# Performance work log

Hardware: AMD Instinct MI355X
Metric: run time of the kernel (lower is better)

## Reference

```python
import jax, jax.numpy as jnp
import numpy as np

B, L, D = 2, 2048, 2048
HEADS, DIM_HEAD = 16, 128
INNER = HEADS * DIM_HEAD
EPS = 1e-6


def _rmsnorm(x, w):
    # RMSNorm over last dim, matching nn.RMSNorm(inner_dim, eps)
    return x * jax.lax.rsqrt(jnp.mean(x * x, axis=-1, keepdims=True) + EPS) * w


def _rope_interleaved(x, cos, sin):
    # x: [B, L, INNER]; cos/sin: [1, L, INNER//2]
    x1 = x[..., 0::2]
    x2 = x[..., 1::2]
    o1 = x1 * cos - x2 * sin
    o2 = x1 * sin + x2 * cos
    return jnp.stack([o1, o2], axis=-1).reshape(x.shape)


def setup_inputs() -> dict:
    key = jax.random.key(0)
    ks = jax.random.split(key, 16)
    s = 0.02
    inp = {
        "x": jax.random.normal(ks[0], (B, L, D), jnp.float32),
        "pe_cos": jax.random.normal(ks[1], (1, L, INNER // 2), jnp.float32),
        "pe_sin": jax.random.normal(ks[2], (1, L, INNER // 2), jnp.float32),
        "logit_log_scale": jax.random.uniform(ks[3], (1, L, 1), jnp.float32),
        "wq": jax.random.normal(ks[4], (D, INNER), jnp.float32) * s,
        "bq": jnp.zeros((INNER,), jnp.float32),
        "wk": jax.random.normal(ks[5], (D, INNER), jnp.float32) * s,
        "bk": jnp.zeros((INNER,), jnp.float32),
        "wv": jax.random.normal(ks[6], (D, INNER), jnp.float32) * s,
        "bv": jnp.zeros((INNER,), jnp.float32),
        "qn_w": jnp.ones((INNER,), jnp.float32),
        "kn_w": jnp.ones((INNER,), jnp.float32),
        "wo": jax.random.normal(ks[7], (INNER, D), jnp.float32) * s,
        "bo": jnp.zeros((D,), jnp.float32),
    }
    return inp


def reference(x, pe_cos, pe_sin, logit_log_scale, wq, bq, wk, bk, wv, bv, qn_w, kn_w, wo, bo):
    # QKV projections
    q = _rmsnorm(x @ wq + bq, qn_w)
    k = _rmsnorm(x @ wk + bk, kn_w)
    v = x @ wv + bv
    # Interleaved RoPE on flattened inner dim
    q = _rope_interleaved(q, pe_cos, pe_sin)
    k = _rope_interleaved(k, pe_cos, pe_sin)
    # Position-dependent logit temperature applied to Q
    q = q * logit_log_scale
    # Split heads: [B, L, H, Dh]
    q = q.reshape(B, L, HEADS, DIM_HEAD)
    k = k.reshape(B, L, HEADS, DIM_HEAD)
    v = v.reshape(B, L, HEADS, DIM_HEAD)
    scale = 1.0 / jnp.sqrt(jnp.asarray(DIM_HEAD, jnp.float32))
    scores = jnp.einsum("bqhd,bkhd->bhqk", q, k) * scale  # [B, H, L, L]
    causal = jnp.tril(jnp.ones((L, L), bool))
    scores = jnp.where(causal[None, None], scores, jnp.asarray(-1e30, scores.dtype))
    attn = jax.nn.softmax(scores, axis=-1)
    out = jnp.einsum("bhqk,bkhd->bqhd", attn, v).reshape(B, L, INNER)
    return out @ wo + bo
```

## Files before the change

kernel.cpp:

```cpp
#include <hip/hip_runtime.h>
#include <hip/hip_bf16.h>

typedef __bf16 bf16x8_t __attribute__((ext_vector_type(8)));
typedef float  f32x4_t  __attribute__((ext_vector_type(4)));

#define B_     2
#define L_     2048
#define D_     2048
#define H_     16
#define DH_    128
#define INNER_ 2048
#define M_     (B_ * L_)

__device__ __forceinline__ void gld_lds16(const void* g, void* l) {
    __builtin_amdgcn_global_load_lds(
        (const __attribute__((address_space(1))) void*)g,
        (__attribute__((address_space(3))) void*)l,
        16, 0, 0);
}

__device__ __forceinline__ unsigned short f2bf(float f) {
    __hip_bfloat16 h = __float2bfloat16(f);
    return *(unsigned short*)&h;
}
__device__ __forceinline__ float bf2f(unsigned short s) {
    return __uint_as_float(((unsigned)s) << 16);
}

__global__ __launch_bounds__(256)
void k_cast(const float* __restrict__ in, unsigned short* __restrict__ out) {
    const size_t i = ((size_t)blockIdx.x * 256 + threadIdx.x) * 4;
    float4 v = *(const float4*)(in + i);
    ushort4 o;
    o.x = f2bf(v.x); o.y = f2bf(v.y); o.z = f2bf(v.z); o.w = f2bf(v.w);
    *(ushort4*)(out + i) = o;
}

__global__ __launch_bounds__(256)
void k_transpose_cast(const float* __restrict__ in, unsigned short* __restrict__ out) {
    __shared__ unsigned short tile[32][33];
    const int t  = threadIdx.x;
    const int r  = t >> 3;
    const int c4 = (t & 7) << 2;
    const size_t ib = ((size_t)blockIdx.y * 32 + r) * 2048 + blockIdx.x * 32 + c4;
    float4 v = *(const float4*)(in + ib);
    tile[r][c4 + 0] = f2bf(v.x); tile[r][c4 + 1] = f2bf(v.y);
    tile[r][c4 + 2] = f2bf(v.z); tile[r][c4 + 3] = f2bf(v.w);
    __syncthreads();
    ushort4 o;
    o.x = tile[c4 + 0][r]; o.y = tile[c4 + 1][r];
    o.z = tile[c4 + 2][r]; o.w = tile[c4 + 3][r];
    const size_t ob = ((size_t)blockIdx.x * 32 + r) * 2048 + blockIdx.y * 32 + c4;
    *(ushort4*)(out + ob) = o;
}

__global__ __launch_bounds__(256)
void k_transpose2048(const unsigned short* __restrict__ in,
                     unsigned short* __restrict__ out) {
    __shared__ unsigned short tile[32][33];
    const int t  = threadIdx.x;
    const int r  = t >> 3;
    const int c4 = (t & 7) << 2;
    const size_t ib = ((size_t)blockIdx.y * 32 + r) * 2048 + blockIdx.x * 32 + c4;
    ushort4 v = *(const ushort4*)(in + ib);
    tile[r][c4 + 0] = v.x; tile[r][c4 + 1] = v.y;
    tile[r][c4 + 2] = v.z; tile[r][c4 + 3] = v.w;
    __syncthreads();
    ushort4 o;
    o.x = tile[c4 + 0][r]; o.y = tile[c4 + 1][r];
    o.z = tile[c4 + 2][r]; o.w = tile[c4 + 3][r];
    const size_t ob = ((size_t)blockIdx.x * 32 + r) * 2048 + blockIdx.y * 32 + c4;
    *(ushort4*)(out + ob) = o;
}

#define GEMM_BODY(A_, Bt_, K_)                                                 \
    __shared__ __align__(16) __hip_bfloat16 As[128 * 32];                      \
    __shared__ __align__(16) __hip_bfloat16 Bs[128 * 32];                      \
    const int t    = threadIdx.x;                                              \
    const int lane = t & 63;                                                   \
    const int wave = t >> 6;                                                   \
    const int quad = lane >> 4;                                                \
    const int l16  = lane & 15;                                                \
    const int wm   = (wave >> 1) * 64;                                         \
    const int wn   = (wave & 1) * 64;                                          \
    const int srow = t >> 2;                                                   \
    const int scol = (t & 3) << 3;                                             \
    const __hip_bfloat16* Ag = A_  + (size_t)(tileM + srow) * K_ + scol;       \
    const __hip_bfloat16* Bg = Bt_ + (size_t)(tileN + srow) * K_ + scol;       \
    __hip_bfloat16* Asl  = &As[t * 8];                                         \
    __hip_bfloat16* Asl2 = &As[2048 + t * 8];                                  \
    __hip_bfloat16* Bsl  = &Bs[t * 8];                                         \
    __hip_bfloat16* Bsl2 = &Bs[2048 + t * 8];                                  \
    const size_t rowskip = (size_t)64 * K_;                                    \
    f32x4_t acc[4][4];                                                         \
    _Pragma("unroll") for (int i = 0; i < 4; i++)                              \
        _Pragma("unroll") for (int j = 0; j < 4; j++)                          \
            acc[i][j] = (f32x4_t){0.f, 0.f, 0.f, 0.f};                         \
    for (int k0 = 0; k0 < K_; k0 += 32) {                                      \
        __syncthreads();                                                       \
        gld_lds16(Ag + k0,           Asl);                                     \
        gld_lds16(Ag + rowskip + k0, Asl2);                                    \
        gld_lds16(Bg + k0,           Bsl);                                     \
        gld_lds16(Bg + rowskip + k0, Bsl2);                                    \
        __syncthreads();                                                       \
        bf16x8_t af[4], bfr[4];                                                \
        _Pragma("unroll") for (int i = 0; i < 4; i++)                          \
            af[i] = *(const bf16x8_t*)&As[(wm + i * 16 + l16) * 32 + quad * 8];\
        _Pragma("unroll") for (int j = 0; j < 4; j++)                          \
            bfr[j] = *(const bf16x8_t*)&Bs[(wn + j * 16 + l16) * 32 + quad * 8];\
        _Pragma("unroll") for (int i = 0; i < 4; i++)                          \
            _Pragma("unroll") for (int j = 0; j < 4; j++)                      \
                acc[i][j] = __builtin_amdgcn_mfma_f32_16x16x32_bf16(           \
                    af[i], bfr[j], acc[i][j], 0, 0, 0);                        \
    }

__global__ __launch_bounds__(256)
void k_gemm_bt_f32(const __hip_bfloat16* __restrict__ A,
                   const __hip_bfloat16* __restrict__ Bt,
                   const float* __restrict__ bias,
                   float* __restrict__ C,
                   int M, int N, int K) {
    const int tileM = blockIdx.x * 128;
    const int tileN = blockIdx.y * 128;
    GEMM_BODY(A, Bt, K)
#pragma unroll
    for (int i = 0; i < 4; i++)
#pragma unroll
        for (int r = 0; r < 4; r++) {
            const int m = tileM + wm + i * 16 + quad * 4 + r;
#pragma unroll
            for (int j = 0; j < 4; j++) {
                const int n = tileN + wn + j * 16 + l16;
                C[(size_t)m * N + n] = acc[i][j][r] + bias[n];
            }
        }
}

__global__ __launch_bounds__(256)
void k_gemm_qkv(const __hip_bfloat16* __restrict__ A,
                const __hip_bfloat16* __restrict__ Bt,
                const float* __restrict__ bq, const float* __restrict__ bk,
                const float* __restrict__ bv,
                __hip_bfloat16* __restrict__ qo, __hip_bfloat16* __restrict__ ko,
                __hip_bfloat16* __restrict__ vo) {
    const int tileM = blockIdx.x * 128;
    const int tileN = blockIdx.y * 128;
    GEMM_BODY(A, Bt, D_)
    const int sel  = blockIdx.y >> 4;
    const int nbas = tileN - sel * INNER_;
    const float* bias = (sel == 0) ? bq : (sel == 1) ? bk : bv;
    __hip_bfloat16* C = (sel == 0) ? qo : (sel == 1) ? ko : vo;
#pragma unroll
    for (int i = 0; i < 4; i++)
#pragma unroll
        for (int r = 0; r < 4; r++) {
            const int m = tileM + wm + i * 16 + quad * 4 + r;
#pragma unroll
            for (int j = 0; j < 4; j++) {
                const int n = nbas + wn + j * 16 + l16;
                C[(size_t)m * INNER_ + n] = __float2bfloat16(acc[i][j][r] + bias[n]);
            }
        }
}

__global__ __launch_bounds__(256)
void k_rmsrope(__hip_bfloat16* __restrict__ buf,
               const float* __restrict__ w,
               const float* __restrict__ pcos,
               const float* __restrict__ psin,
               const float* __restrict__ lls,
               float extra) {
    const int row = blockIdx.x;
    const int l   = row & (L_ - 1);
    const int t   = threadIdx.x;
    __hip_bfloat16* p = buf + (size_t)row * INNER_ + t * 8;

    float x[8];
    {
        const unsigned short* ps = (const unsigned short*)p;
        ushort4 a = *(const ushort4*)ps;
        ushort4 b = *(const ushort4*)(ps + 4);
        unsigned short s[8] = {a.x, a.y, a.z, a.w, b.x, b.y, b.z, b.w};
#pragma unroll
        for (int i = 0; i < 8; i++) x[i] = bf2f(s[i]);
    }
    float ss = 0.f;
#pragma unroll
    for (int i = 0; i < 8; i++) ss += x[i] * x[i];
#pragma unroll
    for (int off = 32; off >= 1; off >>= 1) ss += __shfl_down(ss, off);
    __shared__ float red[4];
    if ((t & 63) == 0) red[t >> 6] = ss;
    __syncthreads();
    ss = red[0] + red[1] + red[2] + red[3];
    const float rstd = rsqrtf(ss * (1.0f / (float)INNER_) + 1e-6f);

    float scale = extra;
    if (lls) scale *= lls[l];

    const float4 c4 = ((const float4*)(pcos + (size_t)l * (INNER_ / 2)))[t];
    const float4 s4 = ((const float4*)(psin + (size_t)l * (INNER_ / 2)))[t];
    const float cc[4] = {c4.x, c4.y, c4.z, c4.w};
    const float sn[4] = {s4.x, s4.y, s4.z, s4.w};
    const float4 w0 = ((const float4*)w)[t * 2];
    const float4 w1 = ((const float4*)w)[t * 2 + 1];
    const float ww[8] = {w0.x, w0.y, w0.z, w0.w, w1.x, w1.y, w1.z, w1.w};

    union { __hip_bfloat16 h[8]; uint4 u; } pk;
#pragma unroll
    for (int pi = 0; pi < 4; pi++) {
        const float y1 = x[pi * 2]     * rstd * ww[pi * 2];
        const float y2 = x[pi * 2 + 1] * rstd * ww[pi * 2 + 1];
        pk.h[pi * 2]     = __float2bfloat16((y1 * cc[pi] - y2 * sn[pi]) * scale);
        pk.h[pi * 2 + 1] = __float2bfloat16((y1 * sn[pi] + y2 * cc[pi]) * scale);
    }
    *(uint4*)p = pk.u;
}

__global__ __launch_bounds__(256)
void k_attn(const __hip_bfloat16* __restrict__ q,
            const __hip_bfloat16* __restrict__ k,
            const __hip_bfloat16* __restrict__ vT,
            __hip_bfloat16* __restrict__ o) {
    __shared__ __align__(16) __hip_bfloat16 Ks[64 * 128];
    __shared__ __align__(16) __hip_bfloat16 Vs[128 * 64];
    __shared__ __align__(16) __hip_bfloat16 Ps[4][16 * 72];

    const int p  = blockIdx.x;
    const int bh = blockIdx.y;
    const int b  = bh >> 4;
    const int h  = bh & 15;
    const int t = threadIdx.x, wave = t >> 6, lane = t & 63;
    const int quad = lane >> 4, l16 = lane & 15;

    const int krow = t >> 4;
    const int kcol = ((t & 15) ^ krow) << 3;
    const int vrow = t >> 3;
    const int vcol = ((t & 7) ^ (vrow & 7)) << 3;

    for (int half = 0; half < 2; ++half) {
        const int qt = half ? (31 - p) : p;

        bf16x8_t aq[4];
        {
            const size_t qoff = (size_t)(b * L_ + qt * 64 + wave * 16 + l16) * INNER_ + h * DH_;
#pragma unroll
            for (int kk = 0; kk < 4; kk++)
                aq[kk] = *(const bf16x8_t*)(q + qoff + kk * 32 + quad * 8);
        }

        f32x4_t oacc[8];
#pragma unroll
        for (int jj = 0; jj < 8; jj++) oacc[jj] = (f32x4_t){0.f, 0.f, 0.f, 0.f};
        float mrow[4] = {-1e30f, -1e30f, -1e30f, -1e30f};
        float lrow[4] = {0.f, 0.f, 0.f, 0.f};

        for (int kt = 0; kt <= qt; ++kt) {
            const int kv0 = kt * 64;
            __syncthreads();
#pragma unroll
            for (int i = 0; i < 4; i++) {
                gld_lds16(k  + (size_t)(b * L_ + kv0 + i * 16 + krow) * INNER_ + h * DH_ + kcol,
                          &Ks[t * 8 + i * 2048]);
                gld_lds16(vT + ((size_t)bh * DH_ + i * 32 + vrow) * L_ + kv0 + vcol,
                          &Vs[t * 8 + i * 2048]);
            }
            __syncthreads();

            f32x4_t sacc[4];
#pragma unroll
            for (int j = 0; j < 4; j++) sacc[j] = (f32x4_t){0.f, 0.f, 0.f, 0.f};
#pragma unroll
            for (int j = 0; j < 4; j++)
#pragma unroll
                for (int kk = 0; kk < 4; kk++) {
                    bf16x8_t bk_ = *(const bf16x8_t*)
                        &Ks[(j * 16 + l16) * 128 + (((kk * 4 + quad) ^ l16) << 3)];
                    sacc[j] = __builtin_amdgcn_mfma_f32_16x16x32_bf16(aq[kk], bk_, sacc[j], 0, 0, 0);
                }

            if (kt == qt) {
                const int qbase = qt * 64 + wave * 16 + quad * 4;
#pragma unroll
                for (int j = 0; j < 4; j++) {
                    const int key = kv0 + j * 16 + l16;
#pragma unroll
                    for (int r = 0; r < 4; r++)
                        if (key > qbase + r) sacc[j][r] = -1e30f;
                }
            }

            float alpha[4];
#pragma unroll
            for (int r = 0; r < 4; r++) {
                float mx = fmaxf(fmaxf(sacc[0][r], sacc[1][r]), fmaxf(sacc[2][r], sacc[3][r]));
#pragma unroll
                for (int off = 1; off < 16; off <<= 1) mx = fmaxf(mx, __shfl_xor(mx, off));
                const float mnew = fmaxf(mrow[r], mx);
                alpha[r] = exp2f(mrow[r] - mnew);
                float s0 = 0.f;
#pragma unroll
                for (int j = 0; j < 4; j++) {
                    const float pv = exp2f(sacc[j][r] - mnew);
                    Ps[wave][(quad * 4 + r) * 72 + j * 16 + l16] = __float2bfloat16(pv);
                    s0 += pv;
                }
#pragma unroll
                for (int off = 1; off < 16; off <<= 1) s0 += __shfl_xor(s0, off);
                lrow[r] = lrow[r] * alpha[r] + s0;
                mrow[r] = mnew;
            }

#pragma unroll
            for (int jj = 0; jj < 8; jj++)
#pragma unroll
                for (int r = 0; r < 4; r++) oacc[jj][r] *= alpha[r];

#pragma unroll
            for (int kk2 = 0; kk2 < 2; kk2++) {
                bf16x8_t ap = *(const bf16x8_t*)&Ps[wave][l16 * 72 + kk2 * 32 + quad * 8];
#pragma unroll
                for (int jj = 0; jj < 8; jj++) {
                    bf16x8_t bv_ = *(const bf16x8_t*)
                        &Vs[(jj * 16 + l16) * 64 + (((kk2 * 4 + quad) ^ (l16 & 7)) << 3)];
                    oacc[jj] = __builtin_amdgcn_mfma_f32_16x16x32_bf16(ap, bv_, oacc[jj], 0, 0, 0);
                }
            }
        }

#pragma unroll
        for (int r = 0; r < 4; r++) {
            const int qi = qt * 64 + wave * 16 + quad * 4 + r;
            const float inv = 1.0f / lrow[r];
#pragma unroll
            for (int jj = 0; jj < 8; jj++) {
                const int d = jj * 16 + l16;
                o[(size_t)(b * L_ + qi) * INNER_ + h * DH_ + d] =
                    __float2bfloat16(oacc[jj][r] * inv);
            }
        }
    }
}

extern "C" void kernel_launch(void* const* d_in, const int* in_sizes, int n_in,
                              void* d_out, int out_size, void* d_ws, size_t ws_size,
                              hipStream_t stream) {
    const float* x      = (const float*)d_in[0];
    const float* pe_cos = (const float*)d_in[1];
    const float* pe_sin = (const float*)d_in[2];
    const float* lls    = (const float*)d_in[3];
    const float* wq     = (const float*)d_in[4];
    const float* bq     = (const float*)d_in[5];
    const float* wk     = (const float*)d_in[6];
    const float* bk     = (const float*)d_in[7];
    const float* wv     = (const float*)d_in[8];
    const float* bv     = (const float*)d_in[9];
    const float* qn     = (const float*)d_in[10];
    const float* kn     = (const float*)d_in[11];
    const float* wo     = (const float*)d_in[12];
    const float* bo     = (const float*)d_in[13];

    char* ws = (char*)d_ws;
    const size_t SZ_W = (size_t)D_ * INNER_ * 2;
    const size_t SZ_M = (size_t)M_ * INNER_ * 2;
    __hip_bfloat16* xb     = (__hip_bfloat16*)ws;  ws += SZ_M;
    __hip_bfloat16* wqkvT  = (__hip_bfloat16*)ws;  ws += 3 * SZ_W;
    __hip_bfloat16* woT    = (__hip_bfloat16*)ws;  ws += SZ_W;
    __hip_bfloat16* qb     = (__hip_bfloat16*)ws;  ws += SZ_M;
    __hip_bfloat16* kb     = (__hip_bfloat16*)ws;  ws += SZ_M;
    __hip_bfloat16* vb     = (__hip_bfloat16*)ws;  ws += SZ_M;
    __hip_bfloat16* vT     = (__hip_bfloat16*)ws;  ws += SZ_M;
    __hip_bfloat16* ab     = (__hip_bfloat16*)ws;  ws += SZ_M;
    (void)in_sizes; (void)n_in; (void)out_size; (void)ws_size;

    const dim3 tb(256);
    const dim3 gT(64, 64);

    k_cast<<<(M_ * D_) / 1024, tb, 0, stream>>>(x, (unsigned short*)xb);

    k_transpose_cast<<<gT, tb, 0, stream>>>(wq, (unsigned short*)(wqkvT));
    k_transpose_cast<<<gT, tb, 0, stream>>>(wk, (unsigned short*)(wqkvT + (size_t)INNER_ * D_));
    k_transpose_cast<<<gT, tb, 0, stream>>>(wv, (unsigned short*)(wqkvT + 2 * (size_t)INNER_ * D_));
    k_transpose_cast<<<gT, tb, 0, stream>>>(wo, (unsigned short*)woT);

    k_gemm_qkv<<<dim3(M_ / 128, 48), tb, 0, stream>>>(xb, wqkvT, bq, bk, bv, qb, kb, vb);

    const float qextra = 0.08838834764831843f  * 1.4426950408889634f ;
    k_rmsrope<<<M_, tb, 0, stream>>>(qb, qn, pe_cos, pe_sin, lls, qextra);
    k_rmsrope<<<M_, tb, 0, stream>>>(kb, kn, pe_cos, pe_sin, nullptr, 1.0f);

    k_transpose2048<<<gT, tb, 0, stream>>>((const unsigned short*)vb, (unsigned short*)vT);
    k_transpose2048<<<gT, tb, 0, stream>>>((const unsigned short*)(vb + (size_t)L_ * INNER_),
                                           (unsigned short*)(vT + (size_t)L_ * INNER_));

    k_attn<<<dim3(16, B_ * H_), tb, 0, stream>>>(qb, kb, vT, ab);

    k_gemm_bt_f32<<<dim3(M_ / 128, D_ / 128), tb, 0, stream>>>(ab, woT, bo, (float*)d_out, M_, D_, INNER_);
}
```

Measured before the change: 476.3 us.

## Enlarge attention query tile to 128 rows with transposed MFMA operand layout

```diff
diff --git a/kernel.cpp b/kernel.cpp
--- a/kernel.cpp
+++ b/kernel.cpp
@@ -224,7 +224,7 @@
             __hip_bfloat16* __restrict__ o) {
     __shared__ __align__(16) __hip_bfloat16 Ks[64 * 128];
     __shared__ __align__(16) __hip_bfloat16 Vs[128 * 64];
-    __shared__ __align__(16) __hip_bfloat16 Ps[4][16 * 72];
+    __shared__ __align__(16) __hip_bfloat16 Pt[8][16 * 72];
 
     const int p  = blockIdx.x;
     const int bh = blockIdx.y;
@@ -233,29 +233,32 @@
     const int t = threadIdx.x, wave = t >> 6, lane = t & 63;
     const int quad = lane >> 4, l16 = lane & 15;
 
-    const int krow = t >> 4;
-    const int kcol = ((t & 15) ^ krow) << 3;
-    const int vrow = t >> 3;
-    const int vcol = ((t & 7) ^ (vrow & 7)) << 3;
+    const int krow = t >> 4, kcol = ((t & 15) ^ krow) << 3;
+    const int vrow = t >> 3, vcol = ((t & 7) ^ (vrow & 7)) << 3;
 
     for (int half = 0; half < 2; ++half) {
-        const int qt = half ? (31 - p) : p;
-
-        bf16x8_t aq[4];
-        {
-            const size_t qoff = (size_t)(b * L_ + qt * 64 + wave * 16 + l16) * INNER_ + h * DH_;
+        const int qt = half ? (15 - p) : p;
+        const int rowbase = qt * 128 + wave * 32;
+
+        bf16x8_t aq[2][4];
+#pragma unroll
+        for (int s = 0; s < 2; s++) {
+            const size_t qoff = (size_t)(b * L_ + rowbase + s * 16 + l16) * INNER_ + h * DH_;
 #pragma unroll
             for (int kk = 0; kk < 4; kk++)
-                aq[kk] = *(const bf16x8_t*)(q + qoff + kk * 32 + quad * 8);
+                aq[s][kk] = *(const bf16x8_t*)(q + qoff + kk * 32 + quad * 8);
         }
 
-        f32x4_t oacc[8];
-#pragma unroll
-        for (int jj = 0; jj < 8; jj++) oacc[jj] = (f32x4_t){0.f, 0.f, 0.f, 0.f};
-        float mrow[4] = {-1e30f, -1e30f, -1e30f, -1e30f};
-        float lrow[4] = {0.f, 0.f, 0.f, 0.f};
-
-        for (int kt = 0; kt <= qt; ++kt) {
+        f32x4_t oacc[2][8];
+#pragma unroll
+        for (int s = 0; s < 2; s++)
+#pragma unroll
+            for (int jj = 0; jj < 8; jj++) oacc[s][jj] = (f32x4_t){0.f, 0.f, 0.f, 0.f};
+        float m_[2] = {-1e30f, -1e30f};
+        float l_[2] = {0.f, 0.f};
+
+        const int nkt = 2 * qt + 2;
+        for (int kt = 0; kt < nkt; ++kt) {
             const int kv0 = kt * 64;
             __syncthreads();
 #pragma unroll
@@ -267,76 +270,98 @@
             }
             __syncthreads();
 
-            f32x4_t sacc[4];
-#pragma unroll
-            for (int j = 0; j < 4; j++) sacc[j] = (f32x4_t){0.f, 0.f, 0.f, 0.f};
-#pragma unroll
-            for (int j = 0; j < 4; j++)
-#pragma unroll
-                for (int kk = 0; kk < 4; kk++) {
-                    bf16x8_t bk_ = *(const bf16x8_t*)
-                        &Ks[(j * 16 + l16) * 128 + (((kk * 4 + quad) ^ l16) << 3)];
-                    sacc[j] = __builtin_amdgcn_mfma_f32_16x16x32_bf16(aq[kk], bk_, sacc[j], 0, 0, 0);
+            if (kv0 > rowbase + 31) continue;
+
+            f32x4_t sacc[2][4];
+#pragma unroll
+            for (int s = 0; s < 2; s++)
+#pragma unroll
+                for (int tt = 0; tt < 4; tt++) sacc[s][tt] = (f32x4_t){0.f, 0.f, 0.f, 0.f};
+#pragma unroll
+            for (int kk = 0; kk < 4; kk++) {
+                bf16x8_t kf[4];
+#pragma unroll
+                for (int tt = 0; tt < 4; tt++)
+                    kf[tt] = *(const bf16x8_t*)&Ks[(tt * 16 + l16) * 128 + (((kk * 4 + quad) ^ l16) << 3)];
+#pragma unroll
+                for (int s = 0; s < 2; s++)
+#pragma unroll
+                    for (int tt = 0; tt < 4; tt++)
+                        sacc[s][tt] = __builtin_amdgcn_mfma_f32_16x16x32_bf16(
+                            kf[tt], aq[s][kk], sacc[s][tt], 0, 0, 0);
+            }
+
+            const bool diag = (kv0 + 63 > rowbase);
+#pragma unroll
+            for (int s = 0; s < 2; s++) {
+                const int sbase = rowbase + s * 16;
+                if (diag) {
+                    const int qrow = sbase + l16;
+#pragma unroll
+                    for (int tt = 0; tt < 4; tt++)
+#pragma unroll
+                        for (int r = 0; r < 4; r++)
+                            if (kv0 + tt * 16 + quad * 4 + r > qrow) sacc[s][tt][r] = -1e30f;
                 }
-
-            if (kt == qt) {
-                const int qbase = qt * 64 + wave * 16 + quad * 4;
-#pragma unroll
-                for (int j = 0; j < 4; j++) {
-                    const int key = kv0 + j * 16 + l16;
-#pragma unroll
-                    for (int r = 0; r < 4; r++)
-                        if (key > qbase + r) sacc[j][r] = -1e30f;
+                float mx = sacc[s][0][0];
+#pragma unroll
+                for (int tt = 0; tt < 4; tt++)
+#pragma unroll
+                    for (int r = 0; r < 4; r++) mx = fmaxf(mx, sacc[s][tt][r]);
+                mx = fmaxf(mx, __shfl_xor(mx, 16));
+                mx = fmaxf(mx, __shfl_xor(mx, 32));
+                const float mnew = fmaxf(m_[s], mx);
+                const float alpha = exp2f(m_[s] - mnew);
+                m_[s] = mnew;
+
+                float ls = 0.f;
+#pragma unroll
+                for (int tt = 0; tt < 4; tt++) {
+                    ushort4 pk;
+                    float p0 = exp2f(sacc[s][tt][0] - mnew);
+                    float p1 = exp2f(sacc[s][tt][1] - mnew);
+                    float p2 = exp2f(sacc[s][tt][2] - mnew);
+                    float p3 = exp2f(sacc[s][tt][3] - mnew);
+                    ls += (p0 + p1) + (p2 + p3);
+                    pk.x = f2bf(p0); pk.y = f2bf(p1); pk.z = f2bf(p2); pk.w = f2bf(p3);
+                    *(ushort4*)&Pt[wave * 2 + s][l16 * 72 + tt * 16 + quad * 4] = pk;
                 }
-            }
-
-            float alpha[4];
-#pragma unroll
-            for (int r = 0; r < 4; r++) {
-                float mx = fmaxf(fmaxf(sacc[0][r], sacc[1][r]), fmaxf(sacc[2][r], sacc[3][r]));
-#pragma unroll
-                for (int off = 1; off < 16; off <<= 1) mx = fmaxf(mx, __shfl_xor(mx, off));
-                const float mnew = fmaxf(mrow[r], mx);
-                alpha[r] = exp2f(mrow[r] - mnew);
-                float s0 = 0.f;
-#pragma unroll
-                for (int j = 0; j < 4; j++) {
-                    const float pv = exp2f(sacc[j][r] - mnew);
-                    Ps[wave][(quad * 4 + r) * 72 + j * 16 + l16] = __float2bfloat16(pv);
-                    s0 += pv;
+                ls += __shfl_xor(ls, 16);
+                ls += __shfl_xor(ls, 32);
+                l_[s] = l_[s] * alpha + ls;
+#pragma unroll
+                for (int jj = 0; jj < 8; jj++) {
+                    oacc[s][jj][0] *= alpha; oacc[s][jj][1] *= alpha;
+                    oacc[s][jj][2] *= alpha; oacc[s][jj][3] *= alpha;
                 }
-#pragma unroll
-                for (int off = 1; off < 16; off <<= 1) s0 += __shfl_xor(s0, off);
-                lrow[r] = lrow[r] * alpha[r] + s0;
-                mrow[r] = mnew;
-            }
-
-#pragma unroll
-            for (int jj = 0; jj < 8; jj++)
-#pragma unroll
-                for (int r = 0; r < 4; r++) oacc[jj][r] *= alpha[r];
+            }
 
 #pragma unroll
             for (int kk2 = 0; kk2 < 2; kk2++) {
-                bf16x8_t ap = *(const bf16x8_t*)&Ps[wave][l16 * 72 + kk2 * 32 + quad * 8];
+                bf16x8_t pf0 = *(const bf16x8_t*)&Pt[wave * 2 + 0][l16 * 72 + kk2 * 32 + quad * 8];
+                bf16x8_t pf1 = *(const bf16x8_t*)&Pt[wave * 2 + 1][l16 * 72 + kk2 * 32 + quad * 8];
 #pragma unroll
                 for (int jj = 0; jj < 8; jj++) {
-                    bf16x8_t bv_ = *(const bf16x8_t*)
+                    bf16x8_t vf = *(const bf16x8_t*)
                         &Vs[(jj * 16 + l16) * 64 + (((kk2 * 4 + quad) ^ (l16 & 7)) << 3)];
-                    oacc[jj] = __builtin_amdgcn_mfma_f32_16x16x32_bf16(ap, bv_, oacc[jj], 0, 0, 0);
+                    oacc[0][jj] = __builtin_amdgcn_mfma_f32_16x16x32_bf16(vf, pf0, oacc[0][jj], 0, 0, 0);
+                    oacc[1][jj] = __builtin_amdgcn_mfma_f32_16x16x32_bf16(vf, pf1, oacc[1][jj], 0, 0, 0);
                 }
             }
         }
 
 #pragma unroll
-        for (int r = 0; r < 4; r++) {
-            const int qi = qt * 64 + wave * 16 + quad * 4 + r;
-            const float inv = 1.0f / lrow[r];
+        for (int s = 0; s < 2; s++) {
+            const float inv = 1.0f / l_[s];
+            __hip_bfloat16* orow = o + (size_t)(b * L_ + rowbase + s * 16 + l16) * INNER_ + h * DH_;
 #pragma unroll
             for (int jj = 0; jj < 8; jj++) {
-                const int d = jj * 16 + l16;
-                o[(size_t)(b * L_ + qi) * INNER_ + h * DH_ + d] =
-                    __float2bfloat16(oacc[jj][r] * inv);
+                ushort4 pk;
+                pk.x = f2bf(oacc[s][jj][0] * inv);
+                pk.y = f2bf(oacc[s][jj][1] * inv);
+                pk.z = f2bf(oacc[s][jj][2] * inv);
+                pk.w = f2bf(oacc[s][jj][3] * inv);
+                *(ushort4*)(orow + jj * 16 + quad * 4) = pk;
             }
         }
     }
@@ -393,7 +418,7 @@
     k_transpose2048<<<gT, tb, 0, stream>>>((const unsigned short*)(vb + (size_t)L_ * INNER_),
                                            (unsigned short*)(vT + (size_t)L_ * INNER_));
 
-    k_attn<<<dim3(16, B_ * H_), tb, 0, stream>>>(qb, kb, vT, ab);
+    k_attn<<<dim3(8, B_ * H_), tb, 0, stream>>>(qb, kb, vT, ab);
 
     k_gemm_bt_f32<<<dim3(M_ / 128, D_ / 128), tb, 0, stream>>>(ab, woT, bo, (float*)d_out, M_, D_, INNER_);
 }
```

New measurement: 458.7 us. 3.7% less time.
